# Optimization experiments

Hardware: AMD Instinct MI355X
Metric: run time of the kernel (lower is better)

Reference implementation:

```python
import jax, jax.numpy as jnp
import numpy as np

B, L, D = 1, 4096, 1024
N_AR, N_DIFF, D_HEAD = 8, 8, 64
H = N_AR + N_DIFF
ROPE_BASE = 10000.0


def rotate_half(x):
    x1, x2 = jnp.split(x, 2, axis=-1)
    return jnp.concatenate([-x2, x1], axis=-1)


def rope_cos_sin(seq_len, d_head):
    inv_freq = 1.0 / (ROPE_BASE ** (jnp.arange(0, d_head, 2, dtype=jnp.float32) / d_head))
    t = jnp.arange(seq_len, dtype=jnp.float32)
    freqs = t[:, None] * inv_freq[None, :]          # [L, d_head//2]
    emb = jnp.concatenate([freqs, freqs], axis=-1)  # [L, d_head]
    return jnp.cos(emb), jnp.sin(emb)


def setup_inputs() -> dict:
    key = jax.random.key(0)
    ks = jax.random.split(key, 5)
    return {
        "hidden_states": jax.random.normal(ks[0], (B, L, D), dtype=jnp.float32),
        "Wq": jax.random.normal(ks[1], (D, H * D_HEAD), dtype=jnp.float32) * 0.02,
        "Wk": jax.random.normal(ks[2], (D, H * D_HEAD), dtype=jnp.float32) * 0.02,
        "Wv": jax.random.normal(ks[3], (D, H * D_HEAD), dtype=jnp.float32) * 0.02,
        "Wo": jax.random.normal(ks[4], (H * D_HEAD, D), dtype=jnp.float32) * 0.02,
    }


def _attend(q, k, v, mask):
    # q,k,v: [B, h, L, d]; mask: [L, L] additive
    scale = D_HEAD ** -0.5
    scores = jnp.einsum("bhqd,bhkd->bhqk", q, k) * scale + mask
    attn = jax.nn.softmax(scores.astype(jnp.float32), axis=-1).astype(q.dtype)
    return jnp.einsum("bhqk,bhkd->bhqd", attn, v)


def reference(hidden_states, Wq, Wk, Wv, Wo):
    b, l, _ = hidden_states.shape

    def heads(x, W):
        return (x @ W).reshape(b, l, H, D_HEAD).transpose(0, 2, 1, 3)  # [B,H,L,d]

    q = heads(hidden_states, Wq)
    k = heads(hidden_states, Wk)
    v = heads(hidden_states, Wv)

    cos, sin = rope_cos_sin(l, D_HEAD)  # [L, d]
    q = q * cos + rotate_half(q) * sin
    k = k * cos + rotate_half(k) * sin

    neg_inf = jnp.finfo(jnp.float32).min
    causal = jnp.where(jnp.tril(jnp.ones((l, l), dtype=bool)), 0.0, -jnp.inf).astype(jnp.float32)

    out_ar = _attend(q[:, :N_AR], k[:, :N_AR], v[:, :N_AR], causal)
    out_diff = _attend(q[:, N_AR:], k[:, N_AR:], v[:, N_AR:], jnp.zeros((l, l), jnp.float32))

    out = jnp.concatenate([out_ar, out_diff], axis=1)          # [B,H,L,d]
    out = out.transpose(0, 2, 1, 3).reshape(b, l, H * D_HEAD)  # [B,L,H*d]
    return out @ Wo
```

## Files before the change

kernel.cpp:

```cpp
#include <hip/hip_runtime.h>

#define LSEQ 4096
#define DMODEL 1024
#define HTOT 16
#define NAR 8
#define DHEAD 64
#define QKVS 3072

typedef unsigned short u16;
typedef unsigned int u32;
typedef __attribute__((ext_vector_type(8))) short bf16x8;
typedef __attribute__((ext_vector_type(4))) short bf16x4;
typedef __attribute__((ext_vector_type(4))) float f32x4;
typedef __attribute__((ext_vector_type(4))) unsigned int u32x4;

typedef __attribute__((address_space(1))) void gvoid;
typedef __attribute__((address_space(3))) void lvoid;

__device__ __forceinline__ void cp16(const void* g, void* l) {
    __builtin_amdgcn_global_load_lds((gvoid*)(void*)g, (lvoid*)l, 16, 0, 0);
}

__device__ __forceinline__ float bfs(u16 v) { return __uint_as_float((u32)v << 16); }
__device__ __forceinline__ u16 f2bf(float f) {
    u32 x = __float_as_uint(f);
    return (u16)((x + 0x7fffu + ((x >> 16) & 1u)) >> 16);
}
__device__ __forceinline__ u32 pack2(float a, float b) {
    return (u32)f2bf(a) | ((u32)f2bf(b) << 16);
}
__device__ __forceinline__ u32 packtr(float lo, float hi) {
    return __builtin_amdgcn_perm(__float_as_uint(hi), __float_as_uint(lo), 0x07060302u);
}

__global__ __launch_bounds__(256) void transp_cvt3(
    const float* __restrict__ Wq, const float* __restrict__ Wk,
    const float* __restrict__ Wv, u16* __restrict__ D)
{
    __shared__ u16 T[64][72];
    const float* S = (blockIdx.z == 0) ? Wq : ((blockIdx.z == 1) ? Wk : Wv);
    u16* Dz = D + (size_t)blockIdx.z * 1024 * 1024;
    const int tid = threadIdx.x;
    const int bx = blockIdx.x, by = blockIdx.y;
#pragma unroll
    for (int i = 0; i < 4; ++i) {
        int id = tid + i * 256;
        int fr = id >> 4, fc = id & 15;
        float4 v = *(const float4*)(S + (size_t)(by * 64 + fr) * 1024 + bx * 64 + fc * 4);
        T[fc * 4 + 0][fr] = f2bf(v.x);
        T[fc * 4 + 1][fr] = f2bf(v.y);
        T[fc * 4 + 2][fr] = f2bf(v.z);
        T[fc * 4 + 3][fr] = f2bf(v.w);
    }
    __syncthreads();
#pragma unroll
    for (int i = 0; i < 2; ++i) {
        int id = tid + i * 256;
        int c = id >> 3, g = id & 7;
        *(uint4*)(Dz + (size_t)(bx * 64 + c) * 1024 + by * 64 + g * 8) = *(const uint4*)&T[c][g * 8];
    }
}

__global__ __launch_bounds__(256) void transp_cvt(
    const float* __restrict__ S, u16* __restrict__ D)
{
    __shared__ u16 T[64][72];
    const int tid = threadIdx.x;
    const int bx = blockIdx.x, by = blockIdx.y;
#pragma unroll
    for (int i = 0; i < 4; ++i) {
        int id = tid + i * 256;
        int fr = id >> 4, fc = id & 15;
        float4 v = *(const float4*)(S + (size_t)(by * 64 + fr) * 1024 + bx * 64 + fc * 4);
        T[fc * 4 + 0][fr] = f2bf(v.x);
        T[fc * 4 + 1][fr] = f2bf(v.y);
        T[fc * 4 + 2][fr] = f2bf(v.z);
        T[fc * 4 + 3][fr] = f2bf(v.w);
    }
    __syncthreads();
#pragma unroll
    for (int i = 0; i < 2; ++i) {
        int id = tid + i * 256;
        int c = id >> 3, g = id & 7;
        *(uint4*)(D + (size_t)(bx * 64 + c) * 1024 + by * 64 + g * 8) = *(const uint4*)&T[c][g * 8];
    }
}

__global__ __launch_bounds__(256) void gemm_qkv(
    const float* __restrict__ A, const u16* __restrict__ Bt, u16* __restrict__ C)
{
    __shared__ u16 As[2][128][40];
    __shared__ u16 Bs[2][128][32];
    const int tid = threadIdx.x;
    const int lane = tid & 63, w = tid >> 6;
    const int col = lane & 15, quad = lane >> 4;
    const int bm = blockIdx.y << 7, bn = blockIdx.x << 7;
    const int wm = (w & 1) << 6, wn = (w >> 1) << 6;
    const int sr = lane >> 2, sc = (lane & 3) << 3;
    const int ar0 = tid >> 2, ag = (tid & 3) << 3;
    const f32x4 zero = {0.f, 0.f, 0.f, 0.f};
    f32x4 acc[4][4];
#pragma unroll
    for (int i = 0; i < 4; ++i)
#pragma unroll
        for (int j = 0; j < 4; ++j) acc[i][j] = zero;

    {
#pragma unroll
        for (int i = 0; i < 2; ++i)
            cp16(Bt + (size_t)(bn + w * 32 + i * 16 + sr) * 1024 + sc, &Bs[0][w * 32 + i * 16][0]);
        float4 a0[2], a1[2];
#pragma unroll
        for (int it = 0; it < 2; ++it) {
            const float* ap = A + (size_t)(bm + ar0 + it * 64) * 1024 + ag;
            a0[it] = *(const float4*)ap;
            a1[it] = *(const float4*)(ap + 4);
        }
#pragma unroll
        for (int it = 0; it < 2; ++it) {
            uint4 pk;
            pk.x = pack2(a0[it].x, a0[it].y); pk.y = pack2(a0[it].z, a0[it].w);
            pk.z = pack2(a1[it].x, a1[it].y); pk.w = pack2(a1[it].z, a1[it].w);
            *(uint4*)&As[0][ar0 + it * 64][ag] = pk;
        }
    }

    for (int kc = 0; kc < 32; ++kc) {
        const int cur = kc & 1, nxt = cur ^ 1;
        __syncthreads();
        const bool pre = (kc + 1 < 32);
        float4 a0[2], a1[2];
        if (pre) {
            const int k1 = (kc + 1) * 32;
#pragma unroll
            for (int i = 0; i < 2; ++i)
                cp16(Bt + (size_t)(bn + w * 32 + i * 16 + sr) * 1024 + k1 + sc,
                     &Bs[nxt][w * 32 + i * 16][0]);
#pragma unroll
            for (int it = 0; it < 2; ++it) {
                const float* ap = A + (size_t)(bm + ar0 + it * 64) * 1024 + k1 + ag;
                a0[it] = *(const float4*)ap;
                a1[it] = *(const float4*)(ap + 4);
            }
        }
        bf16x8 af[4], bfr[4];
#pragma unroll
        for (int i = 0; i < 4; ++i) af[i] = *(const bf16x8*)&As[cur][wm + i * 16 + col][quad * 8];
#pragma unroll
        for (int j = 0; j < 4; ++j) bfr[j] = *(const bf16x8*)&Bs[cur][wn + j * 16 + col][quad * 8];
#pragma unroll
        for (int i = 0; i < 4; ++i)
#pragma unroll
            for (int j = 0; j < 4; ++j)
                acc[i][j] = __builtin_amdgcn_mfma_f32_16x16x32_bf16(af[i], bfr[j], acc[i][j], 0, 0, 0);
        if (pre) {
#pragma unroll
            for (int it = 0; it < 2; ++it) {
                uint4 pk;
                pk.x = pack2(a0[it].x, a0[it].y); pk.y = pack2(a0[it].z, a0[it].w);
                pk.z = pack2(a1[it].x, a1[it].y); pk.w = pack2(a1[it].z, a1[it].w);
                *(uint4*)&As[nxt][ar0 + it * 64][ag] = pk;
            }
        }
    }
#pragma unroll
    for (int i = 0; i < 4; ++i)
#pragma unroll
        for (int j = 0; j < 4; ++j)
#pragma unroll
            for (int r = 0; r < 4; ++r)
                C[(size_t)(bm + wm + i * 16 + quad * 4 + r) * QKVS + bn + wn + j * 16 + col] =
                    f2bf(acc[i][j][r]);
}

__global__ __launch_bounds__(256) void gemm_out(
    const u16* __restrict__ A, const u16* __restrict__ Bt, float* __restrict__ C)
{
    __shared__ u16 As[2][128][32];
    __shared__ u16 Bs[2][128][32];
    const int tid = threadIdx.x;
    const int lane = tid & 63, w = tid >> 6;
    const int col = lane & 15, quad = lane >> 4;
    const int bm = blockIdx.y << 7, bn = blockIdx.x << 7;
    const int wm = (w & 1) << 6, wn = (w >> 1) << 6;
    const int sr = lane >> 2, sc = (lane & 3) << 3;
    const f32x4 zero = {0.f, 0.f, 0.f, 0.f};
    f32x4 acc[4][4];
#pragma unroll
    for (int i = 0; i < 4; ++i)
#pragma unroll
        for (int j = 0; j < 4; ++j) acc[i][j] = zero;

#pragma unroll
    for (int i = 0; i < 2; ++i) {
        const int r0 = w * 32 + i * 16;
        cp16(A  + (size_t)(bm + r0 + sr) * 1024 + sc, &As[0][r0][0]);
        cp16(Bt + (size_t)(bn + r0 + sr) * 1024 + sc, &Bs[0][r0][0]);
    }

    for (int kc = 0; kc < 32; ++kc) {
        const int cur = kc & 1, nxt = cur ^ 1;
        __syncthreads();
        if (kc + 1 < 32) {
            const int k1 = (kc + 1) * 32;
#pragma unroll
            for (int i = 0; i < 2; ++i) {
                const int r0 = w * 32 + i * 16;
                cp16(A  + (size_t)(bm + r0 + sr) * 1024 + k1 + sc, &As[nxt][r0][0]);
                cp16(Bt + (size_t)(bn + r0 + sr) * 1024 + k1 + sc, &Bs[nxt][r0][0]);
            }
        }
        bf16x8 af[4], bfr[4];
#pragma unroll
        for (int i = 0; i < 4; ++i) af[i] = *(const bf16x8*)&As[cur][wm + i * 16 + col][quad * 8];
#pragma unroll
        for (int j = 0; j < 4; ++j) bfr[j] = *(const bf16x8*)&Bs[cur][wn + j * 16 + col][quad * 8];
#pragma unroll
        for (int i = 0; i < 4; ++i)
#pragma unroll
            for (int j = 0; j < 4; ++j)
                acc[i][j] = __builtin_amdgcn_mfma_f32_16x16x32_bf16(af[i], bfr[j], acc[i][j], 0, 0, 0);
    }
#pragma unroll
    for (int i = 0; i < 4; ++i)
#pragma unroll
        for (int j = 0; j < 4; ++j)
#pragma unroll
            for (int r = 0; r < 4; ++r)
                C[(size_t)(bm + wm + i * 16 + quad * 4 + r) * 1024 + bn + wn + j * 16 + col] =
                    acc[i][j][r];
}

__global__ __launch_bounds__(256) void rope_kernel(u16* __restrict__ QKV)
{
    const int idx = blockIdx.x * 256 + threadIdx.x;
    const int i = idx & 31;
    const int h = (idx >> 5) & 15;
    const int t = idx >> 9;
    const float inv = __expf((float)i * -0.2878231366242557f);
    float s, c;
    __sincosf((float)t * inv, &s, &c);
    const size_t base = (size_t)t * QKVS + h * DHEAD + i;
    const float qs = 0.18033688011112042f;

    float q1 = bfs(QKV[base]), q2 = bfs(QKV[base + 32]);
    QKV[base]      = f2bf((q1 * c - q2 * s) * qs);
    QKV[base + 32] = f2bf((q2 * c + q1 * s) * qs);

    const size_t kb = base + 1024;
    float k1 = bfs(QKV[kb]), k2 = bfs(QKV[kb + 32]);
    QKV[kb]      = f2bf(k1 * c - k2 * s);
    QKV[kb + 32] = f2bf(k2 * c + k1 * s);
}

__global__ __launch_bounds__(256) void attn_mfma(
    const u16* __restrict__ QKV, u16* __restrict__ AO)
{
    __shared__ u16 Ks[2][128][64];
    __shared__ u16 Vt[2][64][136];
    const int bid = blockIdx.x;
    int h, qt;
    if (bid < 256) { h = 8 + (bid & 7); qt = bid >> 3; }
    else { int i = bid - 256; h = i & 7; qt = 31 - (i >> 3); }
    const bool causal = (h < NAR);
    const int tid = threadIdx.x;
    const int w = tid >> 6, lane = tid & 63;
    const int col = lane & 15, quad = lane >> 4;
    const int qb = qt * 128;
    const int qr0 = qb + w * 32 + col;
    const int qr1 = qr0 + 16;

    bf16x8 qf[2][2];
#pragma unroll
    for (int s = 0; s < 2; ++s)
#pragma unroll
        for (int ks = 0; ks < 2; ++ks)
            qf[s][ks] = *(const bf16x8*)(QKV + (size_t)(qr0 + s * 16) * QKVS +
                                         h * DHEAD + ks * 32 + quad * 8);

    bf16x4 ones;
    ones[0] = (short)0x3F80; ones[1] = (short)0x3F80;
    ones[2] = (short)0x3F80; ones[3] = (short)0x3F80;

    const f32x4 zero = {0.f, 0.f, 0.f, 0.f};
    f32x4 O[2][5];
#pragma unroll
    for (int s = 0; s < 2; ++s)
#pragma unroll
        for (int nd = 0; nd < 5; ++nd) O[s][nd] = zero;

    const int nch = causal ? (qt + 1) : (LSEQ / 128);
    const int krow = lane >> 3;
    const int kcb = (lane & 7) ^ krow;
    const u16* kbase = QKV + (size_t)krow * QKVS + 1024 + h * DHEAD + kcb * 8;
    const u16* vbase = QKV + (size_t)(lane * 2) * QKVS + 2048 + h * DHEAD + w * 16;

    {
#pragma unroll
        for (int i = 0; i < 4; ++i)
            cp16(kbase + (size_t)((i * 4 + w) * 8) * QKVS, &Ks[0][(i * 4 + w) * 8][0]);
        u32x4 A0 = *(u32x4*)(vbase);
        u32x4 A1 = *(u32x4*)(vbase + 8);
        u32x4 B0 = *(u32x4*)(vbase + QKVS);
        u32x4 B1 = *(u32x4*)(vbase + QKVS + 8);
#pragma unroll
        for (int j = 0; j < 4; ++j) {
            *(u32*)&Vt[0][w * 16 + 2 * j][lane * 2]     = __builtin_amdgcn_perm(B0[j], A0[j], 0x05040100u);
            *(u32*)&Vt[0][w * 16 + 2 * j + 1][lane * 2] = __builtin_amdgcn_perm(B0[j], A0[j], 0x07060302u);
            *(u32*)&Vt[0][w * 16 + 8 + 2 * j][lane * 2]     = __builtin_amdgcn_perm(B1[j], A1[j], 0x05040100u);
            *(u32*)&Vt[0][w * 16 + 8 + 2 * j + 1][lane * 2] = __builtin_amdgcn_perm(B1[j], A1[j], 0x07060302u);
        }
    }

    for (int ch = 0; ch < nch; ++ch) {
        const int cur = ch & 1, nxt = cur ^ 1;
        __syncthreads();
        const bool pre = (ch + 1 < nch);
        u32x4 A0 = {}, A1 = {}, B0 = {}, B1 = {};
        if (pre) {
            const size_t c1 = (size_t)(ch + 1) * 128;
#pragma unroll
            for (int i = 0; i < 4; ++i)
                cp16(kbase + (c1 + (i * 4 + w) * 8) * QKVS, &Ks[nxt][(i * 4 + w) * 8][0]);
            const u16* vp = vbase + c1 * QKVS;
            A0 = *(u32x4*)(vp);
            A1 = *(u32x4*)(vp + 8);
            B0 = *(u32x4*)(vp + QKVS);
            B1 = *(u32x4*)(vp + QKVS + 8);
        }

#pragma unroll
        for (int hf = 0; hf < 2; ++hf) {
            f32x4 st[2][4];
#pragma unroll
            for (int s = 0; s < 2; ++s)
#pragma unroll
                for (int jj = 0; jj < 4; ++jj) st[s][jj] = zero;
#pragma unroll
            for (int jj = 0; jj < 4; ++jj)
#pragma unroll
                for (int ks = 0; ks < 2; ++ks) {
                    bf16x8 kf = *(const bf16x8*)&Ks[cur][(hf * 4 + jj) * 16 + col]
                                                    [((ks * 4 + quad) ^ (col & 7)) * 8];
                    st[0][jj] = __builtin_amdgcn_mfma_f32_16x16x32_bf16(kf, qf[0][ks], st[0][jj], 0, 0, 0);
                    st[1][jj] = __builtin_amdgcn_mfma_f32_16x16x32_bf16(kf, qf[1][ks], st[1][jj], 0, 0, 0);
                }
            if (causal && ch == qt) {
#pragma unroll
                for (int jj = 0; jj < 4; ++jj) {
                    const int kk = ch * 128 + (hf * 4 + jj) * 16 + quad * 4;
#pragma unroll
                    for (int r = 0; r < 4; ++r) {
                        if (kk + r > qr0) st[0][jj][r] = -1e30f;
                        if (kk + r > qr1) st[1][jj][r] = -1e30f;
                    }
                }
            }
            bf16x4 pf[2][4];
#pragma unroll
            for (int s = 0; s < 2; ++s)
#pragma unroll
                for (int jj = 0; jj < 4; ++jj) {
                    u32 lo = packtr(__builtin_amdgcn_exp2f(st[s][jj][0]),
                                    __builtin_amdgcn_exp2f(st[s][jj][1]));
                    u32 hi = packtr(__builtin_amdgcn_exp2f(st[s][jj][2]),
                                    __builtin_amdgcn_exp2f(st[s][jj][3]));
                    u32* p = (u32*)&pf[s][jj];
                    p[0] = lo; p[1] = hi;
                }
#pragma unroll
            for (int nd = 0; nd < 4; ++nd)
#pragma unroll
                for (int jj = 0; jj < 4; ++jj) {
                    bf16x4 vtf = *(const bf16x4*)&Vt[cur][nd * 16 + col][(hf * 4 + jj) * 16 + quad * 4];
                    O[0][nd] = __builtin_amdgcn_mfma_f32_16x16x16bf16_1k(vtf, pf[0][jj], O[0][nd], 0, 0, 0);
                    O[1][nd] = __builtin_amdgcn_mfma_f32_16x16x16bf16_1k(vtf, pf[1][jj], O[1][nd], 0, 0, 0);
                }
#pragma unroll
            for (int jj = 0; jj < 4; ++jj) {
                O[0][4] = __builtin_amdgcn_mfma_f32_16x16x16bf16_1k(ones, pf[0][jj], O[0][4], 0, 0, 0);
                O[1][4] = __builtin_amdgcn_mfma_f32_16x16x16bf16_1k(ones, pf[1][jj], O[1][4], 0, 0, 0);
            }
        }

        if (pre) {
#pragma unroll
            for (int j = 0; j < 4; ++j) {
                *(u32*)&Vt[nxt][w * 16 + 2 * j][lane * 2]     = __builtin_amdgcn_perm(B0[j], A0[j], 0x05040100u);
                *(u32*)&Vt[nxt][w * 16 + 2 * j + 1][lane * 2] = __builtin_amdgcn_perm(B0[j], A0[j], 0x07060302u);
                *(u32*)&Vt[nxt][w * 16 + 8 + 2 * j][lane * 2]     = __builtin_amdgcn_perm(B1[j], A1[j], 0x05040100u);
                *(u32*)&Vt[nxt][w * 16 + 8 + 2 * j + 1][lane * 2] = __builtin_amdgcn_perm(B1[j], A1[j], 0x07060302u);
            }
        }
    }
#pragma unroll
    for (int s = 0; s < 2; ++s) {
        const float inv = 1.f / O[s][4][0];
        const int qrow = qr0 + s * 16;
#pragma unroll
        for (int nd = 0; nd < 4; ++nd) {
            ushort4 ov;
            ov.x = f2bf(O[s][nd][0] * inv);
            ov.y = f2bf(O[s][nd][1] * inv);
            ov.z = f2bf(O[s][nd][2] * inv);
            ov.w = f2bf(O[s][nd][3] * inv);
            *(ushort4*)(AO + (size_t)qrow * 1024 + h * DHEAD + nd * 16 + quad * 4) = ov;
        }
    }
}

extern "C" void kernel_launch(void* const* d_in, const int* in_sizes, int n_in,
                              void* d_out, int out_size, void* d_ws, size_t ws_size,
                              hipStream_t stream)
{
    const float* X  = (const float*)d_in[0];
    const float* Wq = (const float*)d_in[1];
    const float* Wk = (const float*)d_in[2];
    const float* Wv = (const float*)d_in[3];
    const float* Wo = (const float*)d_in[4];
    float* out = (float*)d_out;

    u16* Wt  = (u16*)d_ws;
    u16* AOb = (u16*)d_ws;
    u16* QKV = (u16*)d_ws + (size_t)4 * 1024 * 1024;
    u16* Wot = QKV;

    transp_cvt3<<<dim3(16, 16, 3), 256, 0, stream>>>(Wq, Wk, Wv, Wt);
    gemm_qkv<<<dim3(24, 32), 256, 0, stream>>>(X, Wt, QKV);
    rope_kernel<<<(LSEQ * HTOT * 32) / 256, 256, 0, stream>>>(QKV);
    attn_mfma<<<512, 256, 0, stream>>>(QKV, AOb);
    transp_cvt<<<dim3(16, 16), 256, 0, stream>>>(Wo, Wot);
    gemm_out<<<dim3(8, 32), 256, 0, stream>>>(AOb, Wot, out);
}
```

Measured before the change: 273.0 us.

## Fuse RoPE into QKV GEMM epilogue and software-pipeline attention PV step

Applies rotary embedding and the query scale inside the QKV GEMM epilogue for the Q and K column blocks, which removes the separate rope kernel and its read-modify-write pass over QKV. The attention loop is restructured so the P·V MFMAs for the previous chunk are issued after the next chunk's V transpose and loads, overlapping softmax-exp work with PV matmuls at the cost of holding all 8 P fragments in registers. The A-matrix fp32-to-bf16 conversion now uses truncation via perm instead of round-to-nearest, which is cheaper but less accurate.

```diff
diff --git a/kernel.cpp b/kernel.cpp
--- a/kernel.cpp
+++ b/kernel.cpp
@@ -25,9 +25,6 @@
 __device__ __forceinline__ u16 f2bf(float f) {
     u32 x = __float_as_uint(f);
     return (u16)((x + 0x7fffu + ((x >> 16) & 1u)) >> 16);
-}
-__device__ __forceinline__ u32 pack2(float a, float b) {
-    return (u32)f2bf(a) | ((u32)f2bf(b) << 16);
 }
 __device__ __forceinline__ u32 packtr(float lo, float hi) {
     return __builtin_amdgcn_perm(__float_as_uint(hi), __float_as_uint(lo), 0x07060302u);
@@ -109,18 +106,14 @@
 #pragma unroll
         for (int i = 0; i < 2; ++i)
             cp16(Bt + (size_t)(bn + w * 32 + i * 16 + sr) * 1024 + sc, &Bs[0][w * 32 + i * 16][0]);
-        float4 a0[2], a1[2];
 #pragma unroll
         for (int it = 0; it < 2; ++it) {
             const float* ap = A + (size_t)(bm + ar0 + it * 64) * 1024 + ag;
-            a0[it] = *(const float4*)ap;
-            a1[it] = *(const float4*)(ap + 4);
-        }
-#pragma unroll
-        for (int it = 0; it < 2; ++it) {
+            float4 a0 = *(const float4*)ap;
+            float4 a1 = *(const float4*)(ap + 4);
             uint4 pk;
-            pk.x = pack2(a0[it].x, a0[it].y); pk.y = pack2(a0[it].z, a0[it].w);
-            pk.z = pack2(a1[it].x, a1[it].y); pk.w = pack2(a1[it].z, a1[it].w);
+            pk.x = packtr(a0.x, a0.y); pk.y = packtr(a0.z, a0.w);
+            pk.z = packtr(a1.x, a1.y); pk.w = packtr(a1.z, a1.w);
             *(uint4*)&As[0][ar0 + it * 64][ag] = pk;
         }
     }
@@ -157,11 +150,32 @@
 #pragma unroll
             for (int it = 0; it < 2; ++it) {
                 uint4 pk;
-                pk.x = pack2(a0[it].x, a0[it].y); pk.y = pack2(a0[it].z, a0[it].w);
-                pk.z = pack2(a1[it].x, a1[it].y); pk.w = pack2(a1[it].z, a1[it].w);
+                pk.x = packtr(a0[it].x, a0[it].y); pk.y = packtr(a0[it].z, a0[it].w);
+                pk.z = packtr(a1[it].x, a1[it].y); pk.w = packtr(a1[it].z, a1[it].w);
                 *(uint4*)&As[nxt][ar0 + it * 64][ag] = pk;
             }
         }
+    }
+
+    if (blockIdx.x < 16) {
+        const float scale = (blockIdx.x < 8) ? 0.18033688011112042f : 1.0f;
+        const float inv0 = __expf((float)col * -0.2878231366242557f);
+        const float inv1 = __expf((float)(16 + col) * -0.2878231366242557f);
+#pragma unroll
+        for (int i = 0; i < 4; ++i)
+#pragma unroll
+            for (int r = 0; r < 4; ++r) {
+                const float t = (float)(bm + wm + i * 16 + quad * 4 + r);
+                float s0, c0, s1, c1;
+                __sincosf(t * inv0, &s0, &c0);
+                __sincosf(t * inv1, &s1, &c1);
+                float a0 = acc[i][0][r], b0 = acc[i][2][r];
+                acc[i][0][r] = (a0 * c0 - b0 * s0) * scale;
+                acc[i][2][r] = (b0 * c0 + a0 * s0) * scale;
+                float a1 = acc[i][1][r], b1 = acc[i][3][r];
+                acc[i][1][r] = (a1 * c1 - b1 * s1) * scale;
+                acc[i][3][r] = (b1 * c1 + a1 * s1) * scale;
+            }
     }
 #pragma unroll
     for (int i = 0; i < 4; ++i)
@@ -229,28 +243,6 @@
             for (int r = 0; r < 4; ++r)
                 C[(size_t)(bm + wm + i * 16 + quad * 4 + r) * 1024 + bn + wn + j * 16 + col] =
                     acc[i][j][r];
-}
-
-__global__ __launch_bounds__(256) void rope_kernel(u16* __restrict__ QKV)
-{
-    const int idx = blockIdx.x * 256 + threadIdx.x;
-    const int i = idx & 31;
-    const int h = (idx >> 5) & 15;
-    const int t = idx >> 9;
-    const float inv = __expf((float)i * -0.2878231366242557f);
-    float s, c;
-    __sincosf((float)t * inv, &s, &c);
-    const size_t base = (size_t)t * QKVS + h * DHEAD + i;
-    const float qs = 0.18033688011112042f;
-
-    float q1 = bfs(QKV[base]), q2 = bfs(QKV[base + 32]);
-    QKV[base]      = f2bf((q1 * c - q2 * s) * qs);
-    QKV[base + 32] = f2bf((q2 * c + q1 * s) * qs);
-
-    const size_t kb = base + 1024;
-    float k1 = bfs(QKV[kb]), k2 = bfs(QKV[kb + 32]);
-    QKV[kb]      = f2bf(k1 * c - k2 * s);
-    QKV[kb + 32] = f2bf(k2 * c + k1 * s);
 }
 
 __global__ __launch_bounds__(256) void attn_mfma(
@@ -295,40 +287,112 @@
     const u16* kbase = QKV + (size_t)krow * QKVS + 1024 + h * DHEAD + kcb * 8;
     const u16* vbase = QKV + (size_t)(lane * 2) * QKVS + 2048 + h * DHEAD + w * 16;
 
+    u32x4 vA0, vA1, vB0, vB1;
+    bf16x4 pf[2][8];
+
+#pragma unroll
+    for (int i = 0; i < 4; ++i)
+        cp16(kbase + (size_t)((i * 4 + w) * 8) * QKVS, &Ks[0][(i * 4 + w) * 8][0]);
+    vA0 = *(u32x4*)(vbase);
+    vA1 = *(u32x4*)(vbase + 8);
+    vB0 = *(u32x4*)(vbase + QKVS);
+    vB1 = *(u32x4*)(vbase + QKVS + 8);
+    __syncthreads();
+#pragma unroll
+    for (int j = 0; j < 4; ++j) {
+        *(u32*)&Vt[0][w * 16 + 2 * j][lane * 2]         = __builtin_amdgcn_perm(vB0[j], vA0[j], 0x05040100u);
+        *(u32*)&Vt[0][w * 16 + 2 * j + 1][lane * 2]     = __builtin_amdgcn_perm(vB0[j], vA0[j], 0x07060302u);
+        *(u32*)&Vt[0][w * 16 + 8 + 2 * j][lane * 2]     = __builtin_amdgcn_perm(vB1[j], vA1[j], 0x05040100u);
+        *(u32*)&Vt[0][w * 16 + 8 + 2 * j + 1][lane * 2] = __builtin_amdgcn_perm(vB1[j], vA1[j], 0x07060302u);
+    }
+    if (nch > 1) {
+#pragma unroll
+        for (int i = 0; i < 4; ++i)
+            cp16(kbase + (size_t)(128 + (i * 4 + w) * 8) * QKVS, &Ks[1][(i * 4 + w) * 8][0]);
+        const u16* vp = vbase + (size_t)128 * QKVS;
+        vA0 = *(u32x4*)(vp);
+        vA1 = *(u32x4*)(vp + 8);
+        vB0 = *(u32x4*)(vp + QKVS);
+        vB1 = *(u32x4*)(vp + QKVS + 8);
+    }
     {
-#pragma unroll
-        for (int i = 0; i < 4; ++i)
-            cp16(kbase + (size_t)((i * 4 + w) * 8) * QKVS, &Ks[0][(i * 4 + w) * 8][0]);
-        u32x4 A0 = *(u32x4*)(vbase);
-        u32x4 A1 = *(u32x4*)(vbase + 8);
-        u32x4 B0 = *(u32x4*)(vbase + QKVS);
-        u32x4 B1 = *(u32x4*)(vbase + QKVS + 8);
+        const bool mask = causal && (0 == qt);
+#pragma unroll
+        for (int hf = 0; hf < 2; ++hf) {
+            f32x4 st[2][4];
+#pragma unroll
+            for (int s = 0; s < 2; ++s)
+#pragma unroll
+                for (int jj = 0; jj < 4; ++jj) st[s][jj] = zero;
+#pragma unroll
+            for (int jj = 0; jj < 4; ++jj)
+#pragma unroll
+                for (int ks = 0; ks < 2; ++ks) {
+                    bf16x8 kf = *(const bf16x8*)&Ks[0][(hf * 4 + jj) * 16 + col]
+                                                    [((ks * 4 + quad) ^ (col & 7)) * 8];
+                    st[0][jj] = __builtin_amdgcn_mfma_f32_16x16x32_bf16(kf, qf[0][ks], st[0][jj], 0, 0, 0);
+                    st[1][jj] = __builtin_amdgcn_mfma_f32_16x16x32_bf16(kf, qf[1][ks], st[1][jj], 0, 0, 0);
+                }
+            if (mask) {
+#pragma unroll
+                for (int jj = 0; jj < 4; ++jj) {
+                    const int kk = (hf * 4 + jj) * 16 + quad * 4;
+#pragma unroll
+                    for (int r = 0; r < 4; ++r) {
+                        if (kk + r > qr0) st[0][jj][r] = -1e30f;
+                        if (kk + r > qr1) st[1][jj][r] = -1e30f;
+                    }
+                }
+            }
+#pragma unroll
+            for (int s = 0; s < 2; ++s)
+#pragma unroll
+                for (int jj = 0; jj < 4; ++jj) {
+                    u32 lo = packtr(__builtin_amdgcn_exp2f(st[s][jj][0]),
+                                    __builtin_amdgcn_exp2f(st[s][jj][1]));
+                    u32 hi = packtr(__builtin_amdgcn_exp2f(st[s][jj][2]),
+                                    __builtin_amdgcn_exp2f(st[s][jj][3]));
+                    u32* p = (u32*)&pf[s][hf * 4 + jj];
+                    p[0] = lo; p[1] = hi;
+                }
+        }
+    }
+
+    for (int ch = 1; ch < nch; ++ch) {
+        const int cur = ch & 1, prv = cur ^ 1;
+        __syncthreads();
 #pragma unroll
         for (int j = 0; j < 4; ++j) {
-            *(u32*)&Vt[0][w * 16 + 2 * j][lane * 2]     = __builtin_amdgcn_perm(B0[j], A0[j], 0x05040100u);
-            *(u32*)&Vt[0][w * 16 + 2 * j + 1][lane * 2] = __builtin_amdgcn_perm(B0[j], A0[j], 0x07060302u);
-            *(u32*)&Vt[0][w * 16 + 8 + 2 * j][lane * 2]     = __builtin_amdgcn_perm(B1[j], A1[j], 0x05040100u);
-            *(u32*)&Vt[0][w * 16 + 8 + 2 * j + 1][lane * 2] = __builtin_amdgcn_perm(B1[j], A1[j], 0x07060302u);
-        }
-    }
-
-    for (int ch = 0; ch < nch; ++ch) {
-        const int cur = ch & 1, nxt = cur ^ 1;
-        __syncthreads();
-        const bool pre = (ch + 1 < nch);
-        u32x4 A0 = {}, A1 = {}, B0 = {}, B1 = {};
-        if (pre) {
+            *(u32*)&Vt[cur][w * 16 + 2 * j][lane * 2]         = __builtin_amdgcn_perm(vB0[j], vA0[j], 0x05040100u);
+            *(u32*)&Vt[cur][w * 16 + 2 * j + 1][lane * 2]     = __builtin_amdgcn_perm(vB0[j], vA0[j], 0x07060302u);
+            *(u32*)&Vt[cur][w * 16 + 8 + 2 * j][lane * 2]     = __builtin_amdgcn_perm(vB1[j], vA1[j], 0x05040100u);
+            *(u32*)&Vt[cur][w * 16 + 8 + 2 * j + 1][lane * 2] = __builtin_amdgcn_perm(vB1[j], vA1[j], 0x07060302u);
+        }
+        if (ch + 1 < nch) {
             const size_t c1 = (size_t)(ch + 1) * 128;
 #pragma unroll
             for (int i = 0; i < 4; ++i)
-                cp16(kbase + (c1 + (i * 4 + w) * 8) * QKVS, &Ks[nxt][(i * 4 + w) * 8][0]);
+                cp16(kbase + (c1 + (i * 4 + w) * 8) * QKVS, &Ks[prv][(i * 4 + w) * 8][0]);
             const u16* vp = vbase + c1 * QKVS;
-            A0 = *(u32x4*)(vp);
-            A1 = *(u32x4*)(vp + 8);
-            B0 = *(u32x4*)(vp + QKVS);
-            B1 = *(u32x4*)(vp + QKVS + 8);
-        }
-
+            vA0 = *(u32x4*)(vp);
+            vA1 = *(u32x4*)(vp + 8);
+            vB0 = *(u32x4*)(vp + QKVS);
+            vB1 = *(u32x4*)(vp + QKVS + 8);
+        }
+#pragma unroll
+        for (int nd = 0; nd < 4; ++nd)
+#pragma unroll
+            for (int t = 0; t < 8; ++t) {
+                bf16x4 vtf = *(const bf16x4*)&Vt[prv][nd * 16 + col][t * 16 + quad * 4];
+                O[0][nd] = __builtin_amdgcn_mfma_f32_16x16x16bf16_1k(vtf, pf[0][t], O[0][nd], 0, 0, 0);
+                O[1][nd] = __builtin_amdgcn_mfma_f32_16x16x16bf16_1k(vtf, pf[1][t], O[1][nd], 0, 0, 0);
+            }
+#pragma unroll
+        for (int t = 0; t < 8; ++t) {
+            O[0][4] = __builtin_amdgcn_mfma_f32_16x16x16bf16_1k(ones, pf[0][t], O[0][4], 0, 0, 0);
+            O[1][4] = __builtin_amdgcn_mfma_f32_16x16x16bf16_1k(ones, pf[1][t], O[1][4], 0, 0, 0);
+        }
+        const bool mask = causal && (ch == qt);
 #pragma unroll
         for (int hf = 0; hf < 2; ++hf) {
             f32x4 st[2][4];
@@ -345,7 +409,7 @@
                     st[0][jj] = __builtin_amdgcn_mfma_f32_16x16x32_bf16(kf, qf[0][ks], st[0][jj], 0, 0, 0);
                     st[1][jj] = __builtin_amdgcn_mfma_f32_16x16x32_bf16(kf, qf[1][ks], st[1][jj], 0, 0, 0);
                 }
-            if (causal && ch == qt) {
+            if (mask) {
 #pragma unroll
                 for (int jj = 0; jj < 4; ++jj) {
                     const int kk = ch * 128 + (hf * 4 + jj) * 16 + quad * 4;
@@ -356,7 +420,6 @@
                     }
                 }
             }
-            bf16x4 pf[2][4];
 #pragma unroll
             for (int s = 0; s < 2; ++s)
 #pragma unroll
@@ -365,32 +428,27 @@
                                     __builtin_amdgcn_exp2f(st[s][jj][1]));
                     u32 hi = packtr(__builtin_amdgcn_exp2f(st[s][jj][2]),
                                     __builtin_amdgcn_exp2f(st[s][jj][3]));
-                    u32* p = (u32*)&pf[s][jj];
+                    u32* p = (u32*)&pf[s][hf * 4 + jj];
                     p[0] = lo; p[1] = hi;
                 }
-#pragma unroll
-            for (int nd = 0; nd < 4; ++nd)
-#pragma unroll
-                for (int jj = 0; jj < 4; ++jj) {
-                    bf16x4 vtf = *(const bf16x4*)&Vt[cur][nd * 16 + col][(hf * 4 + jj) * 16 + quad * 4];
-                    O[0][nd] = __builtin_amdgcn_mfma_f32_16x16x16bf16_1k(vtf, pf[0][jj], O[0][nd], 0, 0, 0);
-                    O[1][nd] = __builtin_amdgcn_mfma_f32_16x16x16bf16_1k(vtf, pf[1][jj], O[1][nd], 0, 0, 0);
-                }
-#pragma unroll
-            for (int jj = 0; jj < 4; ++jj) {
-                O[0][4] = __builtin_amdgcn_mfma_f32_16x16x16bf16_1k(ones, pf[0][jj], O[0][4], 0, 0, 0);
-                O[1][4] = __builtin_amdgcn_mfma_f32_16x16x16bf16_1k(ones, pf[1][jj], O[1][4], 0, 0, 0);
-            }
-        }
-
-        if (pre) {
-#pragma unroll
-            for (int j = 0; j < 4; ++j) {
-                *(u32*)&Vt[nxt][w * 16 + 2 * j][lane * 2]     = __builtin_amdgcn_perm(B0[j], A0[j], 0x05040100u);
-                *(u32*)&Vt[nxt][w * 16 + 2 * j + 1][lane * 2] = __builtin_amdgcn_perm(B0[j], A0[j], 0x07060302u);
-                *(u32*)&Vt[nxt][w * 16 + 8 + 2 * j][lane * 2]     = __builtin_amdgcn_perm(B1[j], A1[j], 0x05040100u);
-                *(u32*)&Vt[nxt][w * 16 + 8 + 2 * j + 1][lane * 2] = __builtin_amdgcn_perm(B1[j], A1[j], 0x07060302u);
-            }
+        }
+    }
+
+    __syncthreads();
+    {
+        const int prv = (nch - 1) & 1;
+#pragma unroll
+        for (int nd = 0; nd < 4; ++nd)
+#pragma unroll
+            for (int t = 0; t < 8; ++t) {
+                bf16x4 vtf = *(const bf16x4*)&Vt[prv][nd * 16 + col][t * 16 + quad * 4];
+                O[0][nd] = __builtin_amdgcn_mfma_f32_16x16x16bf16_1k(vtf, pf[0][t], O[0][nd], 0, 0, 0);
+                O[1][nd] = __builtin_amdgcn_mfma_f32_16x16x16bf16_1k(vtf, pf[1][t], O[1][nd], 0, 0, 0);
+            }
+#pragma unroll
+        for (int t = 0; t < 8; ++t) {
+            O[0][4] = __builtin_amdgcn_mfma_f32_16x16x16bf16_1k(ones, pf[0][t], O[0][4], 0, 0, 0);
+            O[1][4] = __builtin_amdgcn_mfma_f32_16x16x16bf16_1k(ones, pf[1][t], O[1][4], 0, 0, 0);
         }
     }
 #pragma unroll
@@ -427,7 +485,6 @@
 
     transp_cvt3<<<dim3(16, 16, 3), 256, 0, stream>>>(Wq, Wk, Wv, Wt);
     gemm_qkv<<<dim3(24, 32), 256, 0, stream>>>(X, Wt, QKV);
-    rope_kernel<<<(LSEQ * HTOT * 32) / 256, 256, 0, stream>>>(QKV);
     attn_mfma<<<512, 256, 0, stream>>>(QKV, AOb);
     transp_cvt<<<dim3(16, 16), 256, 0, stream>>>(Wo, Wot);
     gemm_out<<<dim3(8, 32), 256, 0, stream>>>(AOb, Wot, out);
```

After: 266.1 us. 1.03x faster.
